# Optimization experiments

Measured on AMD Instinct MI355X. Metric: run time of the kernel, lower is better.

## Reference

```python
import math
import jax, jax.numpy as jnp
import numpy as np

B, S, D, H = 4, 2048, 1024, 16
DK = D // H
TINY = 1e-13  # tiny_value_of_dtype(float32) in the original masked_fill


def setup_inputs() -> dict:
    key = jax.random.key(0)
    ks = jax.random.split(key, 12)
    scale = 1.0 / math.sqrt(D)
    inp = {
        "query": jax.random.normal(ks[0], (B, S, D), jnp.float32),
        "key": jax.random.normal(ks[1], (B, S, D), jnp.float32),
        "value": jax.random.normal(ks[2], (B, S, D), jnp.float32),
        "mask": jax.random.randint(ks[3], (B, S, S), 0, 2, jnp.int32),
        "Wq": jax.random.normal(ks[4], (D, D), jnp.float32) * scale,
        "bq": jnp.zeros((D,), jnp.float32),
        "Wk": jax.random.normal(ks[5], (D, D), jnp.float32) * scale,
        "bk": jnp.zeros((D,), jnp.float32),
        "Wv": jax.random.normal(ks[6], (D, D), jnp.float32) * scale,
        "bv": jnp.zeros((D,), jnp.float32),
        "Wo": jax.random.normal(ks[7], (D, D), jnp.float32) * scale,
        "bo": jnp.zeros((D,), jnp.float32),
    }
    return inp


def _split_heads(x):
    # [B, S, D] -> [B, H, S, DK]
    return x.reshape(B, -1, H, DK).transpose(0, 2, 1, 3)


def reference(query, key, value, mask, Wq, bq, Wk, bk, Wv, bv, Wo, bo):
    q = _split_heads(query @ Wq.T + bq)
    k = _split_heads(key @ Wk.T + bk)
    v = _split_heads(value @ Wv.T + bv)
    # scores: [B, H, Sq, Sk]
    scores = jnp.einsum("bhqd,bhkd->bhqk", q, k) / math.sqrt(DK)
    # non-standard mask fill: replace masked positions with TINY (not -inf)
    m = mask[:, None, :, :] == 0  # [B,1,Sq,Sk] broadcast over heads
    scores = jnp.where(m, jnp.float32(TINY), scores)
    p_attn = jax.nn.softmax(scores, axis=-1)
    # dropout is identity in eval/reference mode
    x = jnp.einsum("bhqk,bhkd->bhqd", p_attn, v)
    x = x.transpose(0, 2, 1, 3).reshape(B, -1, D)
    return x @ Wo.T + bo
```

## Files before the change

### kernel.cpp

```cpp
#include <hip/hip_runtime.h>


typedef __attribute__((ext_vector_type(8))) short bf16x8;
typedef __attribute__((ext_vector_type(4))) float f32x4;
typedef __attribute__((ext_vector_type(16))) float f32x16;
typedef __attribute__((ext_vector_type(4))) unsigned short us4;
typedef unsigned long long u64;
typedef unsigned short u16;
typedef unsigned int u32;

#define DEV static __device__ __forceinline__

template <int N> struct IC { static constexpr int v = N; };

DEV u16 f2bf(float f) {
  union { float f; unsigned u; } v; v.f = f;
  return (u16)((v.u + 0x7fffu + ((v.u >> 16) & 1u)) >> 16);
}

DEV u32 cvtpk(float lo, float hi) {
  u32 r;
  asm("v_cvt_pk_bf16_f32 %0, %1, %2" : "=v"(r) : "v"(lo), "v"(hi));
  return r;
}

DEV void plswap(u32& x, u32& y) {
  asm("v_permlane32_swap_b32 %0, %1" : "+v"(x), "+v"(y));
}

DEV float fexp2(float x) {
#if __has_builtin(__builtin_amdgcn_exp2f)
  return __builtin_amdgcn_exp2f(x);
#else
  float r;
  asm volatile("v_exp_f32 %0, %1\n\ts_nop 1" : "=v"(r) : "v"(x));
  return r;
#endif
}

DEV int sbfe1(u32 w, int pos) {
#if __has_builtin(__builtin_amdgcn_sbfe)
  return __builtin_amdgcn_sbfe((int)w, pos, 1);
#else
  return ((int)(w << (31 - pos))) >> 31;
#endif
}

DEV float fmask(float s, int m) {
  union { float f; int i; } u; u.f = s; u.i &= m; return u.f;
}

DEV void gl16(const u16* g, u16* l) {
  __builtin_amdgcn_global_load_lds(
      (const __attribute__((address_space(1))) unsigned int*)g,
      (__attribute__((address_space(3))) unsigned int*)l, 16, 0, 0);
}

DEV int swz(int row, int slot) { return slot ^ (row & 7); }

__global__ void prep_kernel(const float4* __restrict__ q, const float4* __restrict__ k,
                            const float4* __restrict__ v, const float4* __restrict__ wq,
                            const float4* __restrict__ wk, const float4* __restrict__ wv,
                            const float4* __restrict__ wo, const int* __restrict__ mask,
                            us4* __restrict__ xq, us4* __restrict__ xk, us4* __restrict__ xv,
                            us4* __restrict__ owq, us4* __restrict__ owk,
                            us4* __restrict__ owv, us4* __restrict__ owo,
                            u64* __restrict__ bits) {
  const int bid = blockIdx.x;
  if (bid < 28672) {
    const float4* src; us4* dst; int base;
    if (bid < 8192)       { src = q;  dst = xq;  base = 0; }
    else if (bid < 16384) { src = k;  dst = xk;  base = 8192; }
    else if (bid < 24576) { src = v;  dst = xv;  base = 16384; }
    else if (bid < 25600) { src = wq; dst = owq; base = 24576; }
    else if (bid < 26624) { src = wk; dst = owk; base = 25600; }
    else if (bid < 27648) { src = wv; dst = owv; base = 26624; }
    else                  { src = wo; dst = owo; base = 27648; }
    const int i = (bid - base) * 256 + threadIdx.x;
    const float4 t = src[i];
    us4 r = {f2bf(t.x), f2bf(t.y), f2bf(t.z), f2bf(t.w)};
    dst[i] = r;
  } else {
    const int base = (bid - 28672) * 1024 + threadIdx.x;
    int mv[4];
#pragma unroll
    for (int kk = 0; kk < 4; ++kk) mv[kk] = mask[base + kk * 256];
#pragma unroll
    for (int kk = 0; kk < 4; ++kk) {
      const u64 bm = __ballot(mv[kk] != 0);
      if ((threadIdx.x & 63) == 0) bits[(base + kk * 256) >> 6] = bm;
    }
  }
}

template <int MODE>
DEV void gemm_body(const u16* __restrict__ P, const u16* __restrict__ Q,
                   const float* __restrict__ bias, void* __restrict__ outp,
                   int pr0, int qr0, u16* lsP, u16* lsQ) {
  constexpr int K = 1024;
  const int tid = threadIdx.x;
  const int w = tid >> 6, lane = tid & 63;
  const int wm = w >> 1, wn = w & 1;
  const int lo = lane & 15, hi = lane >> 4;
  const int srow = lane >> 3, sslot = lane & 7;

  f32x4 acc[4][4];
#pragma unroll
  for (int i = 0; i < 4; ++i)
#pragma unroll
    for (int j = 0; j < 4; ++j) acc[i][j] = (f32x4){0.f, 0.f, 0.f, 0.f};

  for (int kt = 0; kt < K; kt += 64) {
#pragma unroll
    for (int j = 0; j < 4; ++j) {
      const int c = w * 4 + j;
      const int row = c * 8 + srow;
      const int gs = swz(row, sslot);
      gl16(P + (pr0 + row) * K + kt + gs * 8, &lsP[c * 512]);
      gl16(Q + (qr0 + row) * K + kt + gs * 8, &lsQ[c * 512]);
    }
    __syncthreads();
#pragma unroll
    for (int kk = 0; kk < 2; ++kk) {
      bf16x8 af[4], bfr[4];
#pragma unroll
      for (int mf = 0; mf < 4; ++mf) {
        const int r = wm * 64 + mf * 16 + lo;
        af[mf] = *(const bf16x8*)&lsP[r * 64 + swz(r, kk * 4 + hi) * 8];
      }
#pragma unroll
      for (int nf = 0; nf < 4; ++nf) {
        const int r = wn * 64 + nf * 16 + lo;
        bfr[nf] = *(const bf16x8*)&lsQ[r * 64 + swz(r, kk * 4 + hi) * 8];
      }
#pragma unroll
      for (int mf = 0; mf < 4; ++mf)
#pragma unroll
        for (int nf = 0; nf < 4; ++nf)
          acc[mf][nf] = __builtin_amdgcn_mfma_f32_16x16x32_bf16(af[mf], bfr[nf], acc[mf][nf], 0, 0, 0);
    }
    __syncthreads();
  }

#pragma unroll
  for (int mf = 0; mf < 4; ++mf) {
#pragma unroll
    for (int nf = 0; nf < 4; ++nf) {
#pragma unroll
      for (int i = 0; i < 4; ++i) {
        const int gm = pr0 + wm * 64 + mf * 16 + hi * 4 + i;
        const int gn = qr0 + wn * 64 + nf * 16 + lo;
        float val = acc[mf][nf][i];
        if constexpr (MODE == 0 || MODE == 3) {
          val += bias[gn];
          if constexpr (MODE == 3) val *= 0.18033688011112042f;
          const int b = gm >> 11, s = gm & 2047, h = gn >> 6, dk = gn & 63;
          ((u16*)outp)[(((b * 16 + h) * 2048 + s) * 64) + dk] = f2bf(val);
        } else if constexpr (MODE == 1) {
          val += bias[gm];
          const int h = gm >> 6, dk = gm & 63, b = gn >> 11, s = gn & 2047;
          ((u16*)outp)[(((b * 16 + h) * 64 + dk) * 2048) + s] = f2bf(val);
        } else {
          val += bias[gn];
          ((float*)outp)[(size_t)gm * 1024 + gn] = val;
        }
      }
    }
  }
}

__launch_bounds__(256)
__global__ void gemm_qkv(const u16* __restrict__ xq, const u16* __restrict__ xk,
                         const u16* __restrict__ xv, const u16* __restrict__ wq,
                         const u16* __restrict__ wk, const u16* __restrict__ wv,
                         const float* __restrict__ bq, const float* __restrict__ bk,
                         const float* __restrict__ bv, u16* __restrict__ q16,
                         u16* __restrict__ k16, u16* __restrict__ vt16) {
  __shared__ u16 lsP[128 * 64];
  __shared__ u16 lsQ[128 * 64];
  const int z = blockIdx.z;
  if (z == 0)      gemm_body<3>(xq, wq, bq, q16,  blockIdx.x * 128, blockIdx.y * 128, lsP, lsQ);
  else if (z == 1) gemm_body<0>(xk, wk, bk, k16,  blockIdx.x * 128, blockIdx.y * 128, lsP, lsQ);
  else             gemm_body<1>(wv, xv, bv, vt16, blockIdx.y * 128, blockIdx.x * 128, lsP, lsQ);
}

__launch_bounds__(256)
__global__ void gemm_out(const u16* __restrict__ P, const u16* __restrict__ Q,
                         const float* __restrict__ bias, float* __restrict__ outp) {
  __shared__ u16 lsP[128 * 64];
  __shared__ u16 lsQ[128 * 64];
  gemm_body<2>(P, Q, bias, outp, blockIdx.x * 128, blockIdx.y * 128, lsP, lsQ);
}

__launch_bounds__(256, 4)
__global__ void attn_kernel(const u16* __restrict__ q16, const u16* __restrict__ k16,
                            const u16* __restrict__ vt16, const u64* __restrict__ mb,
                            u16* __restrict__ x16) {
  __shared__ u16 lsK0[64 * 64], lsK1[64 * 64];
  __shared__ u16 lsV0[64 * 64], lsV1[64 * 64];
  const int bh = blockIdx.x;
  const int b = bh >> 4, h = bh & 15;
  const int w = threadIdx.x >> 6, lane = threadIdx.x & 63;
  const int l5 = lane & 31, h1 = lane >> 5, l7 = l5 & 7;
  const int h4 = h1 * 4;
  const int q0 = blockIdx.y * 128 + w * 32;
  const u16* qbase = q16 + (size_t)bh * 2048 * 64;
  const u16* kbase = k16 + (size_t)bh * 2048 * 64;
  const u16* vbase = vt16 + (size_t)bh * 64 * 2048;
  const u64* mp = mb + ((size_t)b * 2048 + q0 + l5) * 32;

  int idx[4];
#pragma unroll
  for (int s4 = 0; s4 < 4; ++s4)
    idx[s4] = l5 * 64 + (((s4 * 2 + h1) ^ l7) * 8);

  const int srow = lane >> 3, sslot = lane & 7;
  const int gs = (sslot ^ srow) * 8;
  const int rowA = w * 16 + srow, rowB = rowA + 8;
  const int dA = w * 1024, dB = w * 1024 + 512;
  const u16* kgA = kbase + rowA * 64 + gs;
  const u16* kgB = kbase + rowB * 64 + gs;
  const u16* vgA = vbase + rowA * 2048 + gs;
  const u16* vgB = vbase + rowB * 2048 + gs;

  const f32x16 z16 = (f32x16)(0.f);

  bf16x8 qf[4];
#pragma unroll
  for (int step = 0; step < 4; ++step)
    qf[step] = *(const bf16x8*)&qbase[(q0 + l5) * 64 + step * 16 + h1 * 8];

  f32x16 acc[2];
  acc[0] = z16; acc[1] = z16;
  float lp0 = 0.f, lp1 = 0.f, lp2 = 0.f, lp3 = 0.f;

  gl16(kgA, &lsK0[dA]); gl16(kgB, &lsK0[dB]);
  gl16(vgA, &lsV0[dA]); gl16(vgB, &lsV0[dB]);
  kgA += 4096; kgB += 4096; vgA += 64; vgB += 64;

  auto body = [&](auto curTag, int t) {
    constexpr int CUR = decltype(curTag)::v;
    const u16* lskR = CUR ? lsK1 : lsK0;
    const u16* lsvR = CUR ? lsV1 : lsV0;
    u16* lskW = CUR ? lsK0 : lsK1;
    u16* lsvW = CUR ? lsV0 : lsV1;

    __syncthreads();

    if (t < 31) {
      gl16(kgA, &lskW[dA]); gl16(kgB, &lskW[dB]);
      gl16(vgA, &lsvW[dA]); gl16(vgB, &lsvW[dB]);
      kgA += 4096; kgB += 4096; vgA += 64; vgB += 64;
    }

    const u64 mw = *mp; ++mp;

    f32x16 s2[2];
    __builtin_amdgcn_s_setprio(1);
#pragma unroll
    for (int f = 0; f < 2; ++f) {
      f32x16 sv = z16;
#pragma unroll
      for (int step = 0; step < 4; ++step) {
        const bf16x8 kf = *(const bf16x8*)&lskR[idx[step] + f * 2048];
        sv = __builtin_amdgcn_mfma_f32_32x32x16_bf16(kf, qf[step], sv, 0, 0, 0);
      }
      s2[f] = sv;
    }
    __builtin_amdgcn_s_setprio(0);

#pragma unroll
    for (int f = 0; f < 2; ++f) {
      const u32 wf = ((f == 0) ? (u32)mw : (u32)(mw >> 32)) >> h4;
      float p[16];
#pragma unroll
      for (int r = 0; r < 16; ++r) {
        const int pos = (r & 3) + 8 * (r >> 2);
        const int m = sbfe1(wf, pos);
        p[r] = fexp2(fmask(s2[f][r], m));
      }
      lp0 += (p[0] + p[4]) + (p[8] + p[12]);
      lp1 += (p[1] + p[5]) + (p[9] + p[13]);
      lp2 += (p[2] + p[6]) + (p[10] + p[14]);
      lp3 += (p[3] + p[7]) + (p[11] + p[15]);
      u32 pk[8];
#pragma unroll
      for (int i = 0; i < 4; ++i) {
        pk[2 * i]     = cvtpk(p[4 * i],     p[4 * i + 1]);
        pk[2 * i + 1] = cvtpk(p[4 * i + 2], p[4 * i + 3]);
      }
      plswap(pk[0], pk[2]); plswap(pk[1], pk[3]);
      plswap(pk[4], pk[6]); plswap(pk[5], pk[7]);

#pragma unroll
      for (int mm = 0; mm < 2; ++mm) {
        const int m = f * 2 + mm;
        union { u32 u[4]; bf16x8 v; } pu;
        pu.u[0] = pk[4 * mm]; pu.u[1] = pk[4 * mm + 1];
        pu.u[2] = pk[4 * mm + 2]; pu.u[3] = pk[4 * mm + 3];
        __builtin_amdgcn_s_setprio(1);
#pragma unroll
        for (int db = 0; db < 2; ++db) {
          const bf16x8 vf = *(const bf16x8*)&lsvR[idx[m] + db * 2048];
          acc[db] = __builtin_amdgcn_mfma_f32_32x32x16_bf16(vf, pu.v, acc[db], 0, 0, 0);
        }
        __builtin_amdgcn_s_setprio(0);
      }
    }
  };

  for (int tt = 0; tt < 16; ++tt) {
    body(IC<0>{}, 2 * tt);
    body(IC<1>{}, 2 * tt + 1);
  }

  const float lpart = (lp0 + lp1) + (lp2 + lp3);
  const float tot = lpart + __shfl_xor(lpart, 32, 64);
  const float inv = 1.0f / tot;

  u16* orow = x16 + ((size_t)b * 2048 + q0 + l5) * 1024 + h * 64;
#pragma unroll
  for (int db = 0; db < 2; ++db)
#pragma unroll
    for (int r = 0; r < 16; r += 2) {
      const int d = db * 32 + (r & 3) + 8 * (r >> 2) + h4;
      *(u32*)&orow[d] = cvtpk(acc[db][r] * inv, acc[db][r + 1] * inv);
    }
}

extern "C" void kernel_launch(void* const* d_in, const int* in_sizes, int n_in,
                              void* d_out, int out_size, void* d_ws, size_t ws_size,
                              hipStream_t stream) {
  const float* query = (const float*)d_in[0];
  const float* key   = (const float*)d_in[1];
  const float* value = (const float*)d_in[2];
  const int*   mask  = (const int*)d_in[3];
  const float* Wq = (const float*)d_in[4];
  const float* bq = (const float*)d_in[5];
  const float* Wk = (const float*)d_in[6];
  const float* bk = (const float*)d_in[7];
  const float* Wv = (const float*)d_in[8];
  const float* bv = (const float*)d_in[9];
  const float* Wo = (const float*)d_in[10];
  const float* bo = (const float*)d_in[11];

  char* ws = (char*)d_ws;
  const size_t MB = 1024 * 1024;
  u16* xq   = (u16*)(ws + 0);
  u16* xk   = (u16*)(ws + 16 * MB);
  u16* xv   = (u16*)(ws + 32 * MB);
  u16* wq16 = (u16*)(ws + 48 * MB);
  u16* wk16 = (u16*)(ws + 50 * MB);
  u16* wv16 = (u16*)(ws + 52 * MB);
  u16* wo16 = (u16*)(ws + 54 * MB);
  u16* q16  = (u16*)(ws + 56 * MB);
  u16* k16  = (u16*)(ws + 72 * MB);
  u16* vt16 = (u16*)(ws + 88 * MB);
  u64* mbits = (u64*)(ws + 104 * MB);
  u16* x16  = xq;

  prep_kernel<<<45056, 256, 0, stream>>>(
      (const float4*)query, (const float4*)key, (const float4*)value,
      (const float4*)Wq, (const float4*)Wk, (const float4*)Wv, (const float4*)Wo,
      mask, (us4*)xq, (us4*)xk, (us4*)xv,
      (us4*)wq16, (us4*)wk16, (us4*)wv16, (us4*)wo16, mbits);

  gemm_qkv<<<dim3(64, 8, 3), 256, 0, stream>>>(xq, xk, xv, wq16, wk16, wv16,
                                               bq, bk, bv, q16, k16, vt16);

  attn_kernel<<<dim3(64, 16), 256, 0, stream>>>(q16, k16, vt16, mbits, x16);

  gemm_out<<<dim3(64, 8), 256, 0, stream>>>(x16, wo16, bo, (float*)d_out);
}
```

Baseline: 221.3 us.

## Software-pipeline attention loop so QK^T of next tile overlaps softmax/PV of previous

Restructures the flash-attention main loop so each iteration computes softmax and PV for the previous K tile while issuing QK^T MFMAs for the current tile. V loads are shifted one stage behind K loads, and a drain step after the loop handles the last tile. The aim is to overlap exp/mask VALU work with matrix-core work and hide LDS latency. The cost is extra live registers for the carried scores (sOld) and the mask word, which may reduce occupancy.

After: 218.5 us (median of 2 runs). No clear change (-1.2%).

```diff
diff --git a/kernel.cpp b/kernel.cpp
--- a/kernel.cpp
+++ b/kernel.cpp
@@ -216,12 +216,11 @@
 
   const int srow = lane >> 3, sslot = lane & 7;
   const int gs = (sslot ^ srow) * 8;
-  const int rowA = w * 16 + srow, rowB = rowA + 8;
+  const int rowA = w * 16 + srow;
   const int dA = w * 1024, dB = w * 1024 + 512;
   const u16* kgA = kbase + rowA * 64 + gs;
-  const u16* kgB = kbase + rowB * 64 + gs;
   const u16* vgA = vbase + rowA * 2048 + gs;
-  const u16* vgB = vbase + rowB * 2048 + gs;
+  const u16* vgB = vbase + (rowA + 8) * 2048 + gs;
 
   const f32x16 z16 = (f32x16)(0.f);
 
@@ -232,57 +231,23 @@
 
   f32x16 acc[2];
   acc[0] = z16; acc[1] = z16;
-  float lp0 = 0.f, lp1 = 0.f, lp2 = 0.f, lp3 = 0.f;
-
-  gl16(kgA, &lsK0[dA]); gl16(kgB, &lsK0[dB]);
-  gl16(vgA, &lsV0[dA]); gl16(vgB, &lsV0[dB]);
-  kgA += 4096; kgB += 4096; vgA += 64; vgB += 64;
-
-  auto body = [&](auto curTag, int t) {
-    constexpr int CUR = decltype(curTag)::v;
-    const u16* lskR = CUR ? lsK1 : lsK0;
-    const u16* lsvR = CUR ? lsV1 : lsV0;
-    u16* lskW = CUR ? lsK0 : lsK1;
-    u16* lsvW = CUR ? lsV0 : lsV1;
-
-    __syncthreads();
-
-    if (t < 31) {
-      gl16(kgA, &lskW[dA]); gl16(kgB, &lskW[dB]);
-      gl16(vgA, &lsvW[dA]); gl16(vgB, &lsvW[dB]);
-      kgA += 4096; kgB += 4096; vgA += 64; vgB += 64;
-    }
-
-    const u64 mw = *mp; ++mp;
-
-    f32x16 s2[2];
-    __builtin_amdgcn_s_setprio(1);
+  f32x16 sOld[2];
+  u64 mwOld = 0;
+  float lp0 = 0.f, lp1 = 0.f;
+
+  auto sm_pv = [&](const u16* lsvR) {
 #pragma unroll
     for (int f = 0; f < 2; ++f) {
-      f32x16 sv = z16;
-#pragma unroll
-      for (int step = 0; step < 4; ++step) {
-        const bf16x8 kf = *(const bf16x8*)&lskR[idx[step] + f * 2048];
-        sv = __builtin_amdgcn_mfma_f32_32x32x16_bf16(kf, qf[step], sv, 0, 0, 0);
-      }
-      s2[f] = sv;
-    }
-    __builtin_amdgcn_s_setprio(0);
-
-#pragma unroll
-    for (int f = 0; f < 2; ++f) {
-      const u32 wf = ((f == 0) ? (u32)mw : (u32)(mw >> 32)) >> h4;
+      const u32 wf = ((f == 0) ? (u32)mwOld : (u32)(mwOld >> 32)) >> h4;
       float p[16];
 #pragma unroll
       for (int r = 0; r < 16; ++r) {
         const int pos = (r & 3) + 8 * (r >> 2);
         const int m = sbfe1(wf, pos);
-        p[r] = fexp2(fmask(s2[f][r], m));
-      }
-      lp0 += (p[0] + p[4]) + (p[8] + p[12]);
-      lp1 += (p[1] + p[5]) + (p[9] + p[13]);
-      lp2 += (p[2] + p[6]) + (p[10] + p[14]);
-      lp3 += (p[3] + p[7]) + (p[11] + p[15]);
+        p[r] = fexp2(fmask(sOld[f][r], m));
+      }
+      lp0 += ((p[0] + p[4]) + (p[8] + p[12])) + ((p[2] + p[6]) + (p[10] + p[14]));
+      lp1 += ((p[1] + p[5]) + (p[9] + p[13])) + ((p[3] + p[7]) + (p[11] + p[15]));
       u32 pk[8];
 #pragma unroll
       for (int i = 0; i < 4; ++i) {
@@ -309,12 +274,53 @@
     }
   };
 
+  gl16(kgA, &lsK0[dA]); gl16(kgA + 512, &lsK0[dB]);
+  kgA += 4096;
+
+  auto body = [&](auto curTag, int t) {
+    constexpr int CUR = decltype(curTag)::v;
+    const u16* lskR = CUR ? lsK1 : lsK0;
+    u16* lskW = CUR ? lsK0 : lsK1;
+    u16* lsvW = CUR ? lsV1 : lsV0;
+    const u16* lsvR = CUR ? lsV0 : lsV1;
+
+    __syncthreads();
+
+    if (t < 31) {
+      gl16(kgA, &lskW[dA]); gl16(kgA + 512, &lskW[dB]);
+      kgA += 4096;
+    }
+    gl16(vgA, &lsvW[dA]); gl16(vgB, &lsvW[dB]);
+    vgA += 64; vgB += 64;
+
+    const u64 mwNew = *mp; ++mp;
+
+    if (t > 0) sm_pv(lsvR);
+    mwOld = mwNew;
+
+    __builtin_amdgcn_s_setprio(1);
+#pragma unroll
+    for (int f = 0; f < 2; ++f) {
+      f32x16 sv = z16;
+#pragma unroll
+      for (int step = 0; step < 4; ++step) {
+        const bf16x8 kf = *(const bf16x8*)&lskR[idx[step] + f * 2048];
+        sv = __builtin_amdgcn_mfma_f32_32x32x16_bf16(kf, qf[step], sv, 0, 0, 0);
+      }
+      sOld[f] = sv;
+    }
+    __builtin_amdgcn_s_setprio(0);
+  };
+
   for (int tt = 0; tt < 16; ++tt) {
     body(IC<0>{}, 2 * tt);
     body(IC<1>{}, 2 * tt + 1);
   }
 
-  const float lpart = (lp0 + lp1) + (lp2 + lp3);
+  __syncthreads();
+  sm_pv(lsV1);
+
+  const float lpart = lp0 + lp1;
   const float tot = lpart + __shfl_xor(lpart, 32, 64);
   const float inv = 1.0f / tot;
 
```
